# Kernel optimization log

Hardware: AMD Instinct MI355X
Metric: run time of the kernel (lower is better)

The kernel has to match this reference:

```python
import jax, jax.numpy as jnp
import numpy as np

B, T, C, H, N = 2, 2048, 2048, 32, 64
EPS_GN = 1e-5 * 8 ** 2  # eps * head_size_divisor^2


def _bf16(t):
    # kernel inputs are cast to bfloat16 in the original module
    return t.astype(jnp.bfloat16).astype(jnp.float32)


def _rwkv7_scan(r, k, v, w, a, b, s0):
    """Generalized delta-rule recurrence (fused_recurrent_rwkv7 semantics).
    r,k,v,w,a,b: [B,T,H,N]; s0: [B,H,N,N] with layout [key, value].
    S_t = diag(exp(w_t)) S + b_t (a_t^T S) + k_t v_t^T ; o_t = r_t^T S_t."""
    def step(S, ts):
        rt, kt, vt, wt, at, bt = ts  # each [B,H,N]
        sa = jnp.einsum('bhk,bhkv->bhv', at, S)
        S = S * jnp.exp(wt)[..., None] + bt[..., None] * sa[..., None, :] + kt[..., None] * vt[..., None, :]
        o = jnp.einsum('bhk,bhkv->bhv', rt, S)
        return S, o
    mv = lambda t: jnp.moveaxis(t, 1, 0)  # [B,T,H,N] -> [T,B,H,N]
    S, o = jax.lax.scan(step, s0, (mv(r), mv(k), mv(v), mv(w), mv(a), mv(b)))
    return jnp.moveaxis(o, 0, 1), S


def _forward(x, shift_state, wkv_state, v_first, x_r, x_w, x_k, x_v, x_a, x_g,
             w0, w1, w2, a0, a1, a2, v0, v1, v2, g1, g2, k_k, k_a, r_k,
             W_r, W_k, W_v, W_o, ln_w, ln_b):
    xx = jnp.concatenate([shift_state[:, None, :], x[:, :-1]], axis=1) - x
    xr, xw, xk, xv, xa, xg = (x + xx * m for m in (x_r, x_w, x_k, x_v, x_a, x_g))
    r = xr @ W_r
    w = -jax.nn.softplus(-(w0 + jnp.tanh(xw @ w1) @ w2)) - 0.5
    k = xk @ W_k
    v = xv @ W_v
    v = v + (v_first - v) * jax.nn.sigmoid(v0 + (xv @ v1) @ v2)  # layer_id > 0 branch
    a = jax.nn.sigmoid(a0 + (xa @ a1) @ a2)
    g = jax.nn.sigmoid(xg @ g1) @ g2
    kk = (k * k_k).reshape(B, T, H, N)
    kk = kk / jnp.maximum(jnp.linalg.norm(kk, axis=-1, keepdims=True), 1e-12)
    kk = kk.reshape(B, T, C)
    k = k * (1.0 + (a - 1.0) * k_a)
    hd = lambda t: _bf16(t).reshape(B, T, H, N)
    o, S = _rwkv7_scan(hd(r), hd(k), hd(v), hd(w), hd(-kk), hd(kk * a), wkv_state)
    y = o.reshape(B, T, H, N)
    # GroupNorm with H groups over C channels
    mu = y.mean(-1, keepdims=True)
    var = ((y - mu) ** 2).mean(-1, keepdims=True)
    y = ((y - mu) / jnp.sqrt(var + EPS_GN)).reshape(B, T, C) * ln_w + ln_b
    rr, k4, vv = r.reshape(B, T, H, N), k.reshape(B, T, H, N), v.reshape(B, T, H, N)
    y = y + ((rr * k4 * r_k).sum(-1, keepdims=True) * vv).reshape(B, T, C)
    out = (y * g) @ W_o
    return out, x[:, -1], S


def setup_inputs() -> dict:
    key = jax.random.key(0)
    ks = iter(jax.random.split(key, 40))
    rn = lambda shape, s=0.02: jax.random.normal(next(ks), shape, jnp.float32) * s
    ru = lambda shape: jax.random.uniform(next(ks), shape, jnp.float32)
    return dict(
        x=rn((B, T, C), 1.0), shift_state=rn((B, C), 1.0),
        wkv_state=jnp.zeros((B, H, N, N), jnp.float32), v_first=rn((B, T, C), 1.0),
        x_r=ru((1, 1, C)), x_w=ru((1, 1, C)), x_k=ru((1, 1, C)),
        x_v=ru((1, 1, C)), x_a=ru((1, 1, C)), x_g=ru((1, 1, C)),
        w0=rn((1, 1, C), 0.5) - 4.0, w1=rn((C, 64)), w2=rn((64, C)),
        a0=jnp.zeros((1, 1, C), jnp.float32), a1=rn((C, 64)), a2=rn((64, C)),
        v0=jnp.ones((1, 1, C), jnp.float32), v1=rn((C, 32)), v2=rn((32, C)),
        g1=rn((C, 128)), g2=rn((128, C)),
        k_k=jnp.full((1, 1, C), 0.85, jnp.float32), k_a=jnp.ones((1, 1, C), jnp.float32),
        r_k=rn((H, N), 0.1),
        W_r=rn((C, C), C ** -0.5), W_k=rn((C, C), C ** -0.5),
        W_v=rn((C, C), C ** -0.5), W_o=rn((C, C), C ** -0.5),
        ln_w=jnp.ones((C,), jnp.float32), ln_b=jnp.zeros((C,), jnp.float32))


def reference(x, shift_state, wkv_state, v_first, x_r, x_w, x_k, x_v, x_a, x_g,
              w0, w1, w2, a0, a1, a2, v0, v1, v2, g1, g2, k_k, k_a, r_k,
              W_r, W_k, W_v, W_o, ln_w, ln_b):
    return _forward(x, shift_state, wkv_state, v_first, x_r, x_w, x_k, x_v, x_a, x_g,
                    w0, w1, w2, a0, a1, a2, v0, v1, v2, g1, g2, k_k, k_a, r_k,
                    W_r, W_k, W_v, W_o, ln_w, ln_b)
```

## Files before the change

kernel.cpp:

```cpp
#include <hip/hip_runtime.h>
#include <cstdint>
#include <cmath>

#define B_ 2
#define T_ 2048
#define C_ 2048
#define H_ 32
#define BT_ (B_ * T_)
#define BTC_ ((size_t)B_ * T_ * C_)
#define L_ 128
#define NC_ 16

typedef __attribute__((ext_vector_type(4))) float f32x4;
typedef __attribute__((ext_vector_type(2))) float f32x2;
typedef __attribute__((ext_vector_type(8))) short bf16x8;
typedef __attribute__((ext_vector_type(4))) unsigned short us4;
typedef __attribute__((ext_vector_type(4))) int i32x4;

__device__ __forceinline__ unsigned short f2bf(float f) {
  union { float f; unsigned int u; } c; c.f = f;
  unsigned int u = c.u;
  return (unsigned short)((u + 0x7FFFu + ((u >> 16) & 1u)) >> 16);
}
__device__ __forceinline__ float bf2f(unsigned short h) {
  union { unsigned int u; float f; } c; c.u = ((unsigned int)h) << 16;
  return c.f;
}
__device__ __forceinline__ float rlane(float v, int lane) {
  return __int_as_float(__builtin_amdgcn_readlane(__float_as_int(v), lane));
}
__device__ __forceinline__ void split4(f32x4 v, us4& h, us4& l) {
  h.x = f2bf(v.x); l.x = f2bf(v.x - bf2f(h.x));
  h.y = f2bf(v.y); l.y = f2bf(v.y - bf2f(h.y));
  h.z = f2bf(v.z); l.z = f2bf(v.z - bf2f(h.z));
  h.w = f2bf(v.w); l.w = f2bf(v.w - bf2f(h.w));
}
__device__ __forceinline__ void g2l(const void* g, void* l) {
  __builtin_amdgcn_global_load_lds((const __attribute__((address_space(1))) void*)g,
                                   (__attribute__((address_space(3))) void*)l, 16, 0, 0);
}

__global__ __launch_bounds__(256) void k_mix(
    const float* __restrict__ x, const float* __restrict__ shift,
    const float* __restrict__ m_r, const float* __restrict__ m_w,
    const float* __restrict__ m_k, const float* __restrict__ m_v,
    const float* __restrict__ m_a, const float* __restrict__ m_g,
    unsigned short* __restrict__ r_h, unsigned short* __restrict__ r_l,
    unsigned short* __restrict__ k_h, unsigned short* __restrict__ k_l,
    unsigned short* __restrict__ v_h, unsigned short* __restrict__ v_l,
    unsigned short* __restrict__ o_w, unsigned short* __restrict__ o_a,
    unsigned short* __restrict__ o_g,
    float* __restrict__ xlast) {
  size_t i4 = ((size_t)blockIdx.x * 256 + threadIdx.x) * 4;
  int c = (int)(i4 % C_);
  size_t bt = i4 / C_;
  int t = (int)(bt % T_);
  int b = (int)(bt / T_);
  f32x4 xv = *(const f32x4*)(x + i4);
  f32x4 pv = (t == 0) ? *(const f32x4*)(shift + (size_t)b * C_ + c)
                      : *(const f32x4*)(x + i4 - C_);
  f32x4 dx = pv - xv;
#define MIXHL(mp, oh, ol) { f32x4 mm = *(const f32x4*)(mp + c); f32x4 rr = xv + dx * mm; \
    us4 hh, ll; split4(rr, hh, ll); *(us4*)(oh + i4) = hh; *(us4*)(ol + i4) = ll; }
#define MIXH(mp, oh) { f32x4 mm = *(const f32x4*)(mp + c); f32x4 rr = xv + dx * mm; \
    us4 pk; pk.x = f2bf(rr.x); pk.y = f2bf(rr.y); pk.z = f2bf(rr.z); pk.w = f2bf(rr.w); \
    *(us4*)(oh + i4) = pk; }
  MIXHL(m_r, r_h, r_l) MIXHL(m_k, k_h, k_l) MIXHL(m_v, v_h, v_l)
  MIXH(m_w, o_w) MIXH(m_a, o_a) MIXH(m_g, o_g)
#undef MIXHL
#undef MIXH
  if (t == T_ - 1) *(f32x4*)(xlast + (size_t)b * C_ + c) = xv;
}

__global__ __launch_bounds__(256) void k_tr(const float* __restrict__ in,
                                            unsigned short* __restrict__ out,
                                            int R, int Cc) {
  __shared__ float tile[32][33];
  int c0 = blockIdx.x * 32, r0 = blockIdx.y * 32;
  int tid = threadIdx.x;
  int rr = tid >> 3, c4 = (tid & 7) * 4;
  f32x4 v = *(const f32x4*)(in + (size_t)(r0 + rr) * Cc + c0 + c4);
  tile[rr][c4] = v.x; tile[rr][c4 + 1] = v.y; tile[rr][c4 + 2] = v.z; tile[rr][c4 + 3] = v.w;
  __syncthreads();
  int cc = tid >> 3, r4 = (tid & 7) * 4;
  us4 o;
  o.x = f2bf(tile[r4][cc]); o.y = f2bf(tile[r4 + 1][cc]);
  o.z = f2bf(tile[r4 + 2][cc]); o.w = f2bf(tile[r4 + 3][cc]);
  *(us4*)(out + (size_t)(c0 + cc) * R + r0 + r4) = o;
}

__global__ __launch_bounds__(256) void k_trs(const float* __restrict__ in,
                                             unsigned short* __restrict__ oh,
                                             unsigned short* __restrict__ ol,
                                             int R, int Cc) {
  __shared__ float tile[32][33];
  int c0 = blockIdx.x * 32, r0 = blockIdx.y * 32;
  int tid = threadIdx.x;
  int rr = tid >> 3, c4 = (tid & 7) * 4;
  f32x4 v = *(const f32x4*)(in + (size_t)(r0 + rr) * Cc + c0 + c4);
  tile[rr][c4] = v.x; tile[rr][c4 + 1] = v.y; tile[rr][c4 + 2] = v.z; tile[rr][c4 + 3] = v.w;
  __syncthreads();
  int cc = tid >> 3, r4 = (tid & 7) * 4;
  f32x4 w = { tile[r4][cc], tile[r4 + 1][cc], tile[r4 + 2][cc], tile[r4 + 3][cc] };
  us4 h, l; split4(w, h, l);
  size_t o = (size_t)(c0 + cc) * R + r0 + r4;
  *(us4*)(oh + o) = h; *(us4*)(ol + o) = l;
}

__global__ __launch_bounds__(256) void k_gemm(
    const unsigned short* __restrict__ X, const unsigned short* __restrict__ Wt,
    void* __restrict__ out, int M, int N, int K, int mode) {
  __shared__ alignas(16) unsigned short As[128 * 32];
  __shared__ alignas(16) unsigned short Bs[128 * 32];
  const int tid = threadIdx.x;
  const int lane = tid & 63, wave = tid >> 6;
  const int wr = wave >> 1, wc = wave & 1;
  const int lm = lane & 15, lq = lane >> 4;
  const int gx = gridDim.x;
  const int nwg = gx * gridDim.y;
  const int bid = blockIdx.y * gx + blockIdx.x;
  const int sz = (bid & 7) * (nwg >> 3) + (bid >> 3);
  const int m0 = (sz / gx) * 128, n0 = (sz % gx) * 128;
  const int srow = (lane >> 2);
  const int kcol = (lane & 3) * 8;
  f32x4 acc[4][4];
#pragma unroll
  for (int i = 0; i < 4; ++i)
#pragma unroll
    for (int j = 0; j < 4; ++j) acc[i][j] = (f32x4){0.f, 0.f, 0.f, 0.f};

  for (int k0 = 0; k0 < K; k0 += 32) {
#pragma unroll
    for (int p = 0; p < 2; ++p) {
      int row = wave * 32 + p * 16 + srow;
      g2l(X + (size_t)(m0 + row) * K + k0 + kcol, As + (wave * 2 + p) * 512);
      int n = n0 + row; if (n > N - 1) n = N - 1;
      g2l(Wt + (size_t)n * K + k0 + kcol, Bs + (wave * 2 + p) * 512);
    }
    __syncthreads();
    bf16x8 af[4], bfr[4];
#pragma unroll
    for (int i = 0; i < 4; ++i)
      af[i] = *(const bf16x8*)(As + (size_t)(wr * 64 + i * 16 + lm) * 32 + lq * 8);
#pragma unroll
    for (int j = 0; j < 4; ++j)
      bfr[j] = *(const bf16x8*)(Bs + (size_t)(wc * 64 + j * 16 + lm) * 32 + lq * 8);
#pragma unroll
    for (int i = 0; i < 4; ++i)
#pragma unroll
      for (int j = 0; j < 4; ++j)
        acc[i][j] = __builtin_amdgcn_mfma_f32_16x16x32_bf16(af[i], bfr[j], acc[i][j], 0, 0, 0);
    __syncthreads();
  }
#pragma unroll
  for (int i = 0; i < 4; ++i)
#pragma unroll
    for (int j = 0; j < 4; ++j) {
      int n = n0 + wc * 64 + j * 16 + lm;
      if (n >= N) continue;
      int mb = m0 + wr * 64 + i * 16 + lq * 4;
#pragma unroll
      for (int r = 0; r < 4; ++r) {
        float val = acc[i][j][r];
        size_t off = (size_t)(mb + r) * N + n;
        if (mode == 0) {
          ((float*)out)[off] = val;
        } else {
          if (mode == 2) val = tanhf(val);
          else if (mode == 3) val = 1.0f / (1.0f + __expf(-val));
          ((unsigned short*)out)[off] = f2bf(val);
        }
      }
    }
}

__global__ __launch_bounds__(256) void k_gemm2(
    const unsigned short* __restrict__ Xh, const unsigned short* __restrict__ Xl, int xlo,
    const unsigned short* __restrict__ Wh, const unsigned short* __restrict__ Wl, int wlo,
    void* __restrict__ out, int M, int N, int K, int mode) {
  __shared__ alignas(16) unsigned short Ah[128 * 32];
  __shared__ alignas(16) unsigned short Al[128 * 32];
  __shared__ alignas(16) unsigned short Bh[128 * 32];
  __shared__ alignas(16) unsigned short Bl[128 * 32];
  const int tid = threadIdx.x;
  const int lane = tid & 63, wave = tid >> 6;
  const int wr = wave >> 1, wc = wave & 1;
  const int lm = lane & 15, lq = lane >> 4;
  const int gx = gridDim.x;
  const int nwg = gx * gridDim.y;
  const int bid = blockIdx.y * gx + blockIdx.x;
  const int sz = (bid & 7) * (nwg >> 3) + (bid >> 3);
  const int m0 = (sz / gx) * 128, n0 = (sz % gx) * 128;
  const int srow = (lane >> 2);
  const int kcol = (lane & 3) * 8;
  f32x4 acc[4][4];
#pragma unroll
  for (int i = 0; i < 4; ++i)
#pragma unroll
    for (int j = 0; j < 4; ++j) acc[i][j] = (f32x4){0.f, 0.f, 0.f, 0.f};

  for (int k0 = 0; k0 < K; k0 += 32) {
#pragma unroll
    for (int p = 0; p < 2; ++p) {
      int row = wave * 32 + p * 16 + srow;
      int off = (wave * 2 + p) * 512;
      size_t ga = (size_t)(m0 + row) * K + k0 + kcol;
      g2l(Xh + ga, Ah + off);
      if (xlo) g2l(Xl + ga, Al + off);
      int n = n0 + row; if (n > N - 1) n = N - 1;
      size_t gb = (size_t)n * K + k0 + kcol;
      g2l(Wh + gb, Bh + off);
      if (wlo) g2l(Wl + gb, Bl + off);
    }
    __syncthreads();
    bf16x8 ah[4], bh[4];
#pragma unroll
    for (int i = 0; i < 4; ++i)
      ah[i] = *(const bf16x8*)(Ah + (size_t)(wr * 64 + i * 16 + lm) * 32 + lq * 8);
#pragma unroll
    for (int j = 0; j < 4; ++j)
      bh[j] = *(const bf16x8*)(Bh + (size_t)(wc * 64 + j * 16 + lm) * 32 + lq * 8);
#pragma unroll
    for (int i = 0; i < 4; ++i)
#pragma unroll
      for (int j = 0; j < 4; ++j)
        acc[i][j] = __builtin_amdgcn_mfma_f32_16x16x32_bf16(ah[i], bh[j], acc[i][j], 0, 0, 0);
    if (xlo) {
      bf16x8 al[4];
#pragma unroll
      for (int i = 0; i < 4; ++i)
        al[i] = *(const bf16x8*)(Al + (size_t)(wr * 64 + i * 16 + lm) * 32 + lq * 8);
#pragma unroll
      for (int i = 0; i < 4; ++i)
#pragma unroll
        for (int j = 0; j < 4; ++j)
          acc[i][j] = __builtin_amdgcn_mfma_f32_16x16x32_bf16(al[i], bh[j], acc[i][j], 0, 0, 0);
    }
    if (wlo) {
      bf16x8 bl[4];
#pragma unroll
      for (int j = 0; j < 4; ++j)
        bl[j] = *(const bf16x8*)(Bl + (size_t)(wc * 64 + j * 16 + lm) * 32 + lq * 8);
#pragma unroll
      for (int i = 0; i < 4; ++i)
#pragma unroll
        for (int j = 0; j < 4; ++j)
          acc[i][j] = __builtin_amdgcn_mfma_f32_16x16x32_bf16(ah[i], bl[j], acc[i][j], 0, 0, 0);
    }
    __syncthreads();
  }
#pragma unroll
  for (int i = 0; i < 4; ++i)
#pragma unroll
    for (int j = 0; j < 4; ++j) {
      int n = n0 + wc * 64 + j * 16 + lm;
      if (n >= N) continue;
      int mb = m0 + wr * 64 + i * 16 + lq * 4;
#pragma unroll
      for (int r = 0; r < 4; ++r) {
        float val = acc[i][j][r];
        size_t off = (size_t)(mb + r) * N + n;
        if (mode == 0) {
          ((float*)out)[off] = val;
        } else {
          if (mode == 2) val = tanhf(val);
          else if (mode == 3) val = 1.0f / (1.0f + __expf(-val));
          ((unsigned short*)out)[off] = f2bf(val);
        }
      }
    }
}

__global__ __launch_bounds__(256) void k_pre(
    const float* __restrict__ rp, const float* __restrict__ kp, float* __restrict__ vp,
    const unsigned short* __restrict__ ww, const unsigned short* __restrict__ aa,
    const unsigned short* __restrict__ vv,
    const float* __restrict__ vfirst,
    const float* __restrict__ w0, const float* __restrict__ a0, const float* __restrict__ v0,
    const float* __restrict__ kkc, const float* __restrict__ kac,
    const float* __restrict__ rkw,
    unsigned short* __restrict__ rb, unsigned short* __restrict__ wb,
    unsigned short* __restrict__ kb, unsigned short* __restrict__ vb,
    unsigned short* __restrict__ ab, unsigned short* __restrict__ bb,
    float* __restrict__ dp) {
  int gw = blockIdx.x * 4 + (threadIdx.x >> 6);
  int l = threadIdx.x & 63;
  int h = gw & (H_ - 1);
  size_t bt = (size_t)(gw >> 5);
  size_t idx = bt * C_ + h * 64 + l;
  int c = h * 64 + l;
  float rf = rp[idx], kf = kp[idx], vr = vp[idx];
  float z = -(w0[c] + bf2f(ww[idx]));
  float sp = (z > 15.f) ? z : log1pf(__expf(z));
  float wv = -sp - 0.5f;
  float ag = 1.f / (1.f + __expf(-(a0[c] + bf2f(aa[idx]))));
  float sv = 1.f / (1.f + __expf(-(v0[c] + bf2f(vv[idx]))));
  float vf = vr + (vfirst[idx] - vr) * sv;
  float kkv = kf * kkc[c];
  float ss = kkv * kkv;
#pragma unroll
  for (int m = 1; m < 64; m <<= 1) ss += __shfl_xor(ss, m);
  float nrm = fmaxf(sqrtf(ss), 1e-12f);
  float kkn = kkv / nrm;
  float ks = kf * (1.f + (ag - 1.f) * kac[c]);
  vp[idx] = vf;
  float bon = rf * ks * rkw[c];
#pragma unroll
  for (int m = 1; m < 64; m <<= 1) bon += __shfl_xor(bon, m);
  if (l == 0) dp[bt * H_ + h] = bon;
  rb[idx] = f2bf(rf); wb[idx] = f2bf(wv); kb[idx] = f2bf(ks);
  vb[idx] = f2bf(vf); ab[idx] = f2bf(-kkn); bb[idx] = f2bf(kkn * ag);
}

__global__ __launch_bounds__(64) void k_scanP(
    const unsigned short* __restrict__ rb,
    const unsigned short* __restrict__ wb, const unsigned short* __restrict__ kb,
    const unsigned short* __restrict__ vb, const unsigned short* __restrict__ ab,
    const unsigned short* __restrict__ bb,
    float* __restrict__ Pg, float* __restrict__ Ug,
    unsigned short* __restrict__ Zg, float* __restrict__ o) {
  const int blk = blockIdx.x;
  const int c = blk & (NC_ - 1), bh = blk >> 4;
  const int b = bh >> 5, h = bh & (H_ - 1);
  const int l = threadIdx.x & 63;
  size_t base = (size_t)b * ((size_t)T_ * C_) + (size_t)(c * L_) * C_ + h * 64 + l;
  size_t zbase = (size_t)blk * 8192;
  float P[64], U[64];
#pragma unroll
  for (int k = 0; k < 64; ++k) { P[k] = (k == l) ? 1.f : 0.f; U[k] = 0.f; }
  float pr[4], pw[4], pk[4], pv[4], pb[4], pa[4];
#pragma unroll
  for (int s = 0; s < 4; ++s) {
    size_t a_ = base + (size_t)s * C_;
    pr[s] = bf2f(rb[a_]); pw[s] = bf2f(wb[a_]); pk[s] = bf2f(kb[a_]);
    pv[s] = bf2f(vb[a_]); pb[s] = bf2f(bb[a_]);
    pa[s] = bf2f(ab[base + (size_t)(s + 1) * C_]);
  }
  float saP = bf2f(ab[base]), saU = 0.f;
  for (int t0 = 0; t0 < L_; t0 += 4) {
#pragma unroll
    for (int u = 0; u < 4; ++u) {
      const int t = t0 + u;
      float rl_ = pr[u], wl = pw[u], kl = pk[u], vl = pv[u], bl = pb[u], al = pa[u];
      if (t + 4 < L_) {
        size_t a_ = base + (size_t)(t + 4) * C_;
        pr[u] = bf2f(rb[a_]); pw[u] = bf2f(wb[a_]); pk[u] = bf2f(kb[a_]);
        pv[u] = bf2f(vb[a_]); pb[u] = bf2f(bb[a_]);
        int ta = t + 5; if (ta > L_ - 1) ta = L_ - 1;
        pa[u] = bf2f(ab[base + (size_t)ta * C_]);
      }
      float ew = exp2f(wl * 1.4426950408889634f);
      float zz0 = 0.f, zz1 = 0.f, zz2 = 0.f, zz3 = 0.f;
      float yy0 = 0.f, yy1 = 0.f, yy2 = 0.f, yy3 = 0.f;
      float qp0 = 0.f, qp1 = 0.f, qp2 = 0.f, qp3 = 0.f;
      float qu0 = 0.f, qu1 = 0.f, qu2 = 0.f, qu3 = 0.f;
#pragma unroll
      for (int k = 0; k < 64; k += 4) {
#define STEPK(kk, ZZ, YY, QP, QU)                                        \
        {                                                                \
          float s_ew = rlane(ew, kk), s_b = rlane(bl, kk),               \
                s_k = rlane(kl, kk);                                     \
          float Pn = fmaf(P[kk], s_ew, s_b * saP);                       \
          float Un = fmaf(U[kk], s_ew, fmaf(s_b, saU, s_k * vl));        \
          P[kk] = Pn; U[kk] = Un;                                        \
          float s_r = rlane(rl_, kk), s_a = rlane(al, kk);               \
          ZZ = fmaf(s_r, Pn, ZZ); YY = fmaf(s_r, Un, YY);                \
          QP = fmaf(s_a, Pn, QP); QU = fmaf(s_a, Un, QU);                \
        }
        STEPK(k,     zz0, yy0, qp0, qu0)
        STEPK(k + 1, zz1, yy1, qp1, qu1)
        STEPK(k + 2, zz2, yy2, qp2, qu2)
        STEPK(k + 3, zz3, yy3, qp3, qu3)
#undef STEPK
      }
      o[base + (size_t)t * C_] = (yy0 + yy1) + (yy2 + yy3);
      Zg[zbase + t * 64 + l] = f2bf((zz0 + zz1) + (zz2 + zz3));
      saP = (qp0 + qp1) + (qp2 + qp3);
      saU = (qu0 + qu1) + (qu2 + qu3);
    }
  }
  size_t pb_ = (size_t)blk * 4096;
#pragma unroll
  for (int k4 = 0; k4 < 64; k4 += 4) {
    f32x4 pv4 = { P[k4], P[k4 + 1], P[k4 + 2], P[k4 + 3] };
    *(f32x4*)(Pg + pb_ + (size_t)l * 64 + k4) = pv4;
  }
#pragma unroll
  for (int k = 0; k < 64; ++k) Ug[pb_ + (size_t)k * 64 + l] = U[k];
}

__global__ __launch_bounds__(256) void k_scanC(
    const float* __restrict__ Pg, const float* __restrict__ Ug,
    const float* __restrict__ s0, float* __restrict__ Scg, float* __restrict__ sout) {
  const int bh = blockIdx.x;
  const int l = threadIdx.x & 63;
  const int kg = __builtin_amdgcn_readfirstlane(threadIdx.x >> 6);
  const int kg16 = kg * 16;
  const int tid = threadIdx.x;
  __shared__ float Sb[4096];
#pragma unroll
  for (int q = 0; q < 4; ++q) {
    int e = tid * 16 + q * 4;
    *(f32x4*)(Sb + e) = *(const f32x4*)(s0 + (size_t)bh * 4096 + e);
  }
  __syncthreads();
  for (int c = 0; c < NC_; ++c) {
    size_t cb = ((size_t)bh * NC_ + c) * 4096;
#pragma unroll
    for (int q = 0; q < 4; ++q) {
      int e = tid * 16 + q * 4;
      *(f32x4*)(Scg + cb + e) = *(const f32x4*)(Sb + e);
    }
    const float* Pt = Pg + cb;
    const float* Uc = Ug + cb;
    float acc[16];
#pragma unroll
    for (int i = 0; i < 16; ++i) acc[i] = Uc[(size_t)(kg16 + i) * 64 + l];
    for (int j = 0; j < 64; ++j) {
      float s = Sb[j * 64 + l];
#pragma unroll
      for (int i = 0; i < 16; ++i) acc[i] = fmaf(Pt[j * 64 + kg16 + i], s, acc[i]);
    }
    __syncthreads();
#pragma unroll
    for (int i = 0; i < 16; ++i) Sb[(kg16 + i) * 64 + l] = acc[i];
    __syncthreads();
  }
#pragma unroll
  for (int q = 0; q < 4; ++q) {
    int e = tid * 16 + q * 4;
    *(f32x4*)(sout + (size_t)bh * 4096 + e) = *(const f32x4*)(Sb + e);
  }
}

__global__ __launch_bounds__(256) void k_scanO(
    const unsigned short* __restrict__ Zg, const float* __restrict__ Scg,
    float* __restrict__ o) {
  const int blk = blockIdx.x;
  const int c = blk & (NC_ - 1), bh = blk >> 4;
  const int b = bh >> 5, h = bh & (H_ - 1);
  const int l = threadIdx.x & 63;
  const int w = threadIdx.x >> 6;
  float S[64];
  const float* Sp = Scg + (size_t)blk * 4096 + l;
#pragma unroll
  for (int k = 0; k < 64; ++k) S[k] = Sp[(size_t)k * 64];
  size_t zb = (size_t)blk * 8192;
  size_t ob = (size_t)b * ((size_t)T_ * C_) + (size_t)(c * L_) * C_ + h * 64 + l;
  for (int tt = 0; tt < 32; ++tt) {
    int t = w * 32 + tt;
    float zv = bf2f(Zg[zb + t * 64 + l]);
    float a0_ = 0.f, a1_ = 0.f, a2_ = 0.f, a3_ = 0.f;
#pragma unroll
    for (int k = 0; k < 64; k += 4) {
      a0_ = fmaf(rlane(zv, k), S[k], a0_);
      a1_ = fmaf(rlane(zv, k + 1), S[k + 1], a1_);
      a2_ = fmaf(rlane(zv, k + 2), S[k + 2], a2_);
      a3_ = fmaf(rlane(zv, k + 3), S[k + 3], a3_);
    }
    o[ob + (size_t)t * C_] += (a0_ + a1_) + (a2_ + a3_);
  }
}

__global__ __launch_bounds__(256) void k_post(
    const float* __restrict__ o, const float* __restrict__ vp, const float* __restrict__ gp,
    const float* __restrict__ dp,
    const float* __restrict__ lnw, const float* __restrict__ lnb,
    unsigned short* __restrict__ z) {
  int gw = blockIdx.x * 4 + (threadIdx.x >> 6);
  int l = threadIdx.x & 63;
  int h = gw & (H_ - 1);
  size_t bt = (size_t)(gw >> 5);
  size_t idx = bt * C_ + h * 64 + l;
  int c = h * 64 + l;
  float ov = o[idx];
  float s1 = ov;
#pragma unroll
  for (int m = 1; m < 64; m <<= 1) s1 += __shfl_xor(s1, m);
  float mu = s1 * (1.f / 64.f);
  float d = ov - mu;
  float s2 = d * d;
#pragma unroll
  for (int m = 1; m < 64; m <<= 1) s2 += __shfl_xor(s2, m);
  float var = s2 * (1.f / 64.f);
  float y = d * rsqrtf(var + 6.4e-4f);
  y = y * lnw[c] + lnb[c];
  y = fmaf(dp[bt * H_ + h], vp[idx], y);
  z[idx] = f2bf(y * gp[idx]);
}

extern "C" void kernel_launch(void* const* d_in, const int* in_sizes, int n_in,
                              void* d_out, int out_size, void* d_ws, size_t ws_size,
                              hipStream_t stream) {
  const float* x      = (const float*)d_in[0];
  const float* shift  = (const float*)d_in[1];
  const float* wkv    = (const float*)d_in[2];
  const float* vfirst = (const float*)d_in[3];
  const float* x_r    = (const float*)d_in[4];
  const float* x_w    = (const float*)d_in[5];
  const float* x_k    = (const float*)d_in[6];
  const float* x_v    = (const float*)d_in[7];
  const float* x_a    = (const float*)d_in[8];
  const float* x_g    = (const float*)d_in[9];
  const float* w0     = (const float*)d_in[10];
  const float* w1     = (const float*)d_in[11];
  const float* w2     = (const float*)d_in[12];
  const float* a0     = (const float*)d_in[13];
  const float* a1     = (const float*)d_in[14];
  const float* a2     = (const float*)d_in[15];
  const float* v0     = (const float*)d_in[16];
  const float* v1     = (const float*)d_in[17];
  const float* v2     = (const float*)d_in[18];
  const float* g1     = (const float*)d_in[19];
  const float* g2     = (const float*)d_in[20];
  const float* k_k    = (const float*)d_in[21];
  const float* k_a    = (const float*)d_in[22];
  const float* r_k    = (const float*)d_in[23];
  const float* W_r    = (const float*)d_in[24];
  const float* W_k    = (const float*)d_in[25];
  const float* W_v    = (const float*)d_in[26];
  const float* W_o    = (const float*)d_in[27];
  const float* ln_w   = (const float*)d_in[28];
  const float* ln_b   = (const float*)d_in[29];

  char* wp = (char*)d_ws;
  auto alloc = [&](size_t bytes) { char* p = wp; wp += (bytes + 255) & ~(size_t)255; return p; };
  const size_t SB = BTC_ * 2;
  const size_t SF = BTC_ * 4;

  unsigned short* w1t = (unsigned short*)alloc((size_t)C_ * 64 * 2);
  unsigned short* w2t = (unsigned short*)alloc((size_t)C_ * 64 * 2);
  unsigned short* a1t = (unsigned short*)alloc((size_t)C_ * 64 * 2);
  unsigned short* a2t = (unsigned short*)alloc((size_t)C_ * 64 * 2);
  unsigned short* v1t = (unsigned short*)alloc((size_t)C_ * 32 * 2);
  unsigned short* v2t = (unsigned short*)alloc((size_t)C_ * 32 * 2);
  unsigned short* g1t = (unsigned short*)alloc((size_t)C_ * 128 * 2);
  unsigned short* g2t = (unsigned short*)alloc((size_t)C_ * 128 * 2);
  unsigned short* hw  = (unsigned short*)alloc((size_t)BT_ * 64 * 2);
  unsigned short* ha  = (unsigned short*)alloc((size_t)BT_ * 64 * 2);
  unsigned short* hv  = (unsigned short*)alloc((size_t)BT_ * 32 * 2);
  unsigned short* hg  = (unsigned short*)alloc((size_t)BT_ * 128 * 2);
  unsigned short* Wt2 = (unsigned short*)alloc((size_t)C_ * C_ * 2 * 2);
  float* dp           = (float*)alloc((size_t)BT_ * H_ * 4);
  unsigned short* xw  = (unsigned short*)alloc(SB);
  unsigned short* xa  = (unsigned short*)alloc(SB);
  unsigned short* xg  = (unsigned short*)alloc(SB);
  unsigned short* xr2 = (unsigned short*)alloc(2 * SB);
  unsigned short* xk2 = (unsigned short*)alloc(2 * SB);
  unsigned short* xv2 = (unsigned short*)alloc(2 * SB);
  float* rbuf         = (float*)alloc(SF);
  unsigned short* vbb = (unsigned short*)alloc(SB);

  unsigned short* Wh = Wt2;
  unsigned short* Wl = Wt2 + (size_t)C_ * C_;
  unsigned short* xr_h = xr2, *xr_l = xr2 + BTC_;
  unsigned short* xk_h = xk2, *xk_l = xk2 + BTC_;
  unsigned short* xv_h = xv2, *xv_l = xv2 + BTC_;
  float* kbuf = (float*)xr2;
  float* vbuf = (float*)xk2;
  unsigned short* rb = xv2;
  unsigned short* kb = xv2 + BTC_;
  float* gfull = rbuf;
  unsigned short* zbuf = (unsigned short*)xr2;
  float* Pg  = (float*)xr2;
  float* Ug  = Pg + (size_t)1024 * 4096;
  unsigned short* zg = Wt2;
  float* Scg = (float*)xw;

  float* outp  = (float*)d_out;
  float* xlast = outp + BTC_;
  float* soutp = outp + BTC_ + (size_t)B_ * C_;
  float* obuf  = outp;

  auto tr = [&](const float* in, unsigned short* out, int R, int Cc) {
    k_tr<<<dim3(Cc / 32, R / 32), 256, 0, stream>>>(in, out, R, Cc);
  };
  auto gemm = [&](const unsigned short* X, const unsigned short* Wtp, void* out,
                  int M, int N, int K, int mode) {
    k_gemm<<<dim3((N + 127) / 128, M / 128), 256, 0, stream>>>(X, Wtp, out, M, N, K, mode);
  };
  auto gemm2 = [&](const unsigned short* Xh_, const unsigned short* Xl_, int xlo,
                   const unsigned short* Wh_, const unsigned short* Wl_, int wlo,
                   void* out, int M, int N, int K, int mode) {
    k_gemm2<<<dim3((N + 127) / 128, M / 128), 256, 0, stream>>>(Xh_, Xl_, xlo, Wh_, Wl_, wlo,
                                                                out, M, N, K, mode);
  };

  k_mix<<<(int)(BTC_ / 4 / 256), 256, 0, stream>>>(x, shift, x_r, x_w, x_k, x_v, x_a, x_g,
                                                   xr_h, xr_l, xk_h, xk_l, xv_h, xv_l,
                                                   xw, xa, xg, xlast);
  tr(w1, w1t, C_, 64);  tr(w2, w2t, 64, C_);
  tr(a1, a1t, C_, 64);  tr(a2, a2t, 64, C_);
  tr(v1, v1t, C_, 32);  tr(v2, v2t, 32, C_);
  tr(g1, g1t, C_, 128); tr(g2, g2t, 128, C_);

  gemm(xw, w1t, hw, BT_, 64, C_, 2);
  gemm(xa, a1t, ha, BT_, 64, C_, 1);
  gemm2(xv_h, xv_l, 1, v1t, nullptr, 0, hv, BT_, 32, C_, 1);
  gemm(xg, g1t, hg, BT_, 128, C_, 3);

  k_trs<<<dim3(C_ / 32, C_ / 32), 256, 0, stream>>>(W_r, Wh, Wl, C_, C_);
  gemm2(xr_h, xr_l, 1, Wh, Wl, 1, rbuf, BT_, C_, C_, 0);
  k_trs<<<dim3(C_ / 32, C_ / 32), 256, 0, stream>>>(W_k, Wh, Wl, C_, C_);
  gemm2(xk_h, xk_l, 1, Wh, Wl, 1, kbuf, BT_, C_, C_, 0);
  k_trs<<<dim3(C_ / 32, C_ / 32), 256, 0, stream>>>(W_v, Wh, Wl, C_, C_);
  gemm2(xv_h, xv_l, 1, Wh, Wl, 1, vbuf, BT_, C_, C_, 0);

  gemm(hw, w2t, xw, BT_, C_, 64, 1);
  gemm(ha, a2t, xa, BT_, C_, 64, 1);
  gemm(hv, v2t, xg, BT_, C_, 32, 1);

  k_pre<<<BT_ * H_ / 4, 256, 0, stream>>>(rbuf, kbuf, vbuf, xw, xa, xg, vfirst,
                                          w0, a0, v0, k_k, k_a, r_k,
                                          rb, xw, kb, vbb, xa, xg, dp);

  gemm(hg, g2t, gfull, BT_, C_, 128, 0);

  k_scanP<<<B_ * H_ * NC_, 64, 0, stream>>>(rb, xw, kb, vbb, xa, xg, Pg, Ug, zg, obuf);
  k_scanC<<<B_ * H_, 256, 0, stream>>>(Pg, Ug, wkv, Scg, soutp);
  k_scanO<<<B_ * H_ * NC_, 256, 0, stream>>>(zg, Scg, obuf);

  k_post<<<BT_ * H_ / 4, 256, 0, stream>>>(obuf, vbuf, gfull, dp, ln_w, ln_b, zbuf);

  tr(W_o, Wh, C_, C_);
  gemm(zbuf, Wh, outp, BT_, C_, C_, 0);
}
```

Baseline: 1.408 ms.

## Halve scan chunk length, store P in bf16, split chunk combine across column blocks

```diff
diff --git a/kernel.cpp b/kernel.cpp
--- a/kernel.cpp
+++ b/kernel.cpp
@@ -8,8 +8,8 @@
 #define H_ 32
 #define BT_ (B_ * T_)
 #define BTC_ ((size_t)B_ * T_ * C_)
-#define L_ 128
-#define NC_ 16
+#define L_ 64
+#define NC_ 32
 
 typedef __attribute__((ext_vector_type(4))) float f32x4;
 typedef __attribute__((ext_vector_type(2))) float f32x2;
@@ -317,14 +317,14 @@
     const unsigned short* __restrict__ wb, const unsigned short* __restrict__ kb,
     const unsigned short* __restrict__ vb, const unsigned short* __restrict__ ab,
     const unsigned short* __restrict__ bb,
-    float* __restrict__ Pg, float* __restrict__ Ug,
+    unsigned short* __restrict__ Pg, float* __restrict__ Ug,
     unsigned short* __restrict__ Zg, float* __restrict__ o) {
   const int blk = blockIdx.x;
-  const int c = blk & (NC_ - 1), bh = blk >> 4;
+  const int c = blk & (NC_ - 1), bh = blk / NC_;
   const int b = bh >> 5, h = bh & (H_ - 1);
   const int l = threadIdx.x & 63;
   size_t base = (size_t)b * ((size_t)T_ * C_) + (size_t)(c * L_) * C_ + h * 64 + l;
-  size_t zbase = (size_t)blk * 8192;
+  size_t zbase = (size_t)blk * (L_ * 64);
   float P[64], U[64];
 #pragma unroll
   for (int k = 0; k < 64; ++k) { P[k] = (k == l) ? 1.f : 0.f; U[k] = 0.f; }
@@ -382,62 +382,79 @@
   size_t pb_ = (size_t)blk * 4096;
 #pragma unroll
   for (int k4 = 0; k4 < 64; k4 += 4) {
-    f32x4 pv4 = { P[k4], P[k4 + 1], P[k4 + 2], P[k4 + 3] };
-    *(f32x4*)(Pg + pb_ + (size_t)l * 64 + k4) = pv4;
+    us4 pk4;
+    pk4.x = f2bf(P[k4]); pk4.y = f2bf(P[k4 + 1]);
+    pk4.z = f2bf(P[k4 + 2]); pk4.w = f2bf(P[k4 + 3]);
+    *(us4*)(Pg + pb_ + (size_t)l * 64 + k4) = pk4;
   }
 #pragma unroll
   for (int k = 0; k < 64; ++k) Ug[pb_ + (size_t)k * 64 + l] = U[k];
 }
 
 __global__ __launch_bounds__(256) void k_scanC(
-    const float* __restrict__ Pg, const float* __restrict__ Ug,
+    const unsigned short* __restrict__ Pg, const float* __restrict__ Ug,
     const float* __restrict__ s0, float* __restrict__ Scg, float* __restrict__ sout) {
-  const int bh = blockIdx.x;
-  const int l = threadIdx.x & 63;
-  const int kg = __builtin_amdgcn_readfirstlane(threadIdx.x >> 6);
-  const int kg16 = kg * 16;
+  const int bh = blockIdx.x >> 2, q = blockIdx.x & 3;
   const int tid = threadIdx.x;
-  __shared__ float Sb[4096];
-#pragma unroll
-  for (int q = 0; q < 4; ++q) {
-    int e = tid * 16 + q * 4;
-    *(f32x4*)(Sb + e) = *(const f32x4*)(s0 + (size_t)bh * 4096 + e);
+  const int col = tid & 15;
+  const int r0 = (tid >> 4) * 4;
+  const int colg = q * 16 + col;
+  __shared__ float Sb[64][16];
+  __shared__ alignas(16) unsigned short Pb[4096];
+  float sreg[4];
+#pragma unroll
+  for (int rr = 0; rr < 4; ++rr) {
+    float v = s0[(size_t)bh * 4096 + (r0 + rr) * 64 + colg];
+    sreg[rr] = v; Sb[r0 + rr][col] = v;
+  }
+  {
+    size_t cb0 = ((size_t)bh * NC_) * 4096;
+    *(us4*)(Pb + tid * 16)      = *(const us4*)(Pg + cb0 + tid * 16);
+    *(us4*)(Pb + tid * 16 + 4)  = *(const us4*)(Pg + cb0 + tid * 16 + 4);
+    *(us4*)(Pb + tid * 16 + 8)  = *(const us4*)(Pg + cb0 + tid * 16 + 8);
+    *(us4*)(Pb + tid * 16 + 12) = *(const us4*)(Pg + cb0 + tid * 16 + 12);
   }
   __syncthreads();
   for (int c = 0; c < NC_; ++c) {
     size_t cb = ((size_t)bh * NC_ + c) * 4096;
 #pragma unroll
-    for (int q = 0; q < 4; ++q) {
-      int e = tid * 16 + q * 4;
-      *(f32x4*)(Scg + cb + e) = *(const f32x4*)(Sb + e);
-    }
-    const float* Pt = Pg + cb;
-    const float* Uc = Ug + cb;
-    float acc[16];
-#pragma unroll
-    for (int i = 0; i < 16; ++i) acc[i] = Uc[(size_t)(kg16 + i) * 64 + l];
+    for (int rr = 0; rr < 4; ++rr)
+      Scg[cb + (size_t)(r0 + rr) * 64 + colg] = sreg[rr];
+    float acc0 = Ug[cb + (size_t)r0 * 64 + colg];
+    float acc1 = Ug[cb + (size_t)(r0 + 1) * 64 + colg];
+    float acc2 = Ug[cb + (size_t)(r0 + 2) * 64 + colg];
+    float acc3 = Ug[cb + (size_t)(r0 + 3) * 64 + colg];
     for (int j = 0; j < 64; ++j) {
-      float s = Sb[j * 64 + l];
-#pragma unroll
-      for (int i = 0; i < 16; ++i) acc[i] = fmaf(Pt[j * 64 + kg16 + i], s, acc[i]);
+      float s = Sb[j][col];
+      us4 p4 = *(const us4*)(Pb + j * 64 + r0);
+      acc0 = fmaf(bf2f(p4.x), s, acc0);
+      acc1 = fmaf(bf2f(p4.y), s, acc1);
+      acc2 = fmaf(bf2f(p4.z), s, acc2);
+      acc3 = fmaf(bf2f(p4.w), s, acc3);
     }
     __syncthreads();
-#pragma unroll
-    for (int i = 0; i < 16; ++i) Sb[(kg16 + i) * 64 + l] = acc[i];
+    Sb[r0][col] = acc0; Sb[r0 + 1][col] = acc1;
+    Sb[r0 + 2][col] = acc2; Sb[r0 + 3][col] = acc3;
+    sreg[0] = acc0; sreg[1] = acc1; sreg[2] = acc2; sreg[3] = acc3;
+    if (c + 1 < NC_) {
+      size_t cbn = cb + 4096;
+      *(us4*)(Pb + tid * 16)      = *(const us4*)(Pg + cbn + tid * 16);
+      *(us4*)(Pb + tid * 16 + 4)  = *(const us4*)(Pg + cbn + tid * 16 + 4);
+      *(us4*)(Pb + tid * 16 + 8)  = *(const us4*)(Pg + cbn + tid * 16 + 8);
+      *(us4*)(Pb + tid * 16 + 12) = *(const us4*)(Pg + cbn + tid * 16 + 12);
+    }
     __syncthreads();
   }
 #pragma unroll
-  for (int q = 0; q < 4; ++q) {
-    int e = tid * 16 + q * 4;
-    *(f32x4*)(sout + (size_t)bh * 4096 + e) = *(const f32x4*)(Sb + e);
-  }
+  for (int rr = 0; rr < 4; ++rr)
+    sout[(size_t)bh * 4096 + (r0 + rr) * 64 + colg] = sreg[rr];
 }
 
 __global__ __launch_bounds__(256) void k_scanO(
     const unsigned short* __restrict__ Zg, const float* __restrict__ Scg,
     float* __restrict__ o) {
   const int blk = blockIdx.x;
-  const int c = blk & (NC_ - 1), bh = blk >> 4;
+  const int c = blk & (NC_ - 1), bh = blk / NC_;
   const int b = bh >> 5, h = bh & (H_ - 1);
   const int l = threadIdx.x & 63;
   const int w = threadIdx.x >> 6;
@@ -445,10 +462,10 @@
   const float* Sp = Scg + (size_t)blk * 4096 + l;
 #pragma unroll
   for (int k = 0; k < 64; ++k) S[k] = Sp[(size_t)k * 64];
-  size_t zb = (size_t)blk * 8192;
+  size_t zb = (size_t)blk * (L_ * 64);
   size_t ob = (size_t)b * ((size_t)T_ * C_) + (size_t)(c * L_) * C_ + h * 64 + l;
-  for (int tt = 0; tt < 32; ++tt) {
-    int t = w * 32 + tt;
+  for (int tt = 0; tt < L_ / 4; ++tt) {
+    int t = w * (L_ / 4) + tt;
     float zv = bf2f(Zg[zb + t * 64 + l]);
     float a0_ = 0.f, a1_ = 0.f, a2_ = 0.f, a3_ = 0.f;
 #pragma unroll
@@ -463,7 +480,8 @@
 }
 
 __global__ __launch_bounds__(256) void k_post(
-    const float* __restrict__ o, const float* __restrict__ vp, const float* __restrict__ gp,
+    const float* __restrict__ o, const float* __restrict__ vp,
+    const unsigned short* __restrict__ gp,
     const float* __restrict__ dp,
     const float* __restrict__ lnw, const float* __restrict__ lnb,
     unsigned short* __restrict__ z) {
@@ -486,7 +504,7 @@
   float y = d * rsqrtf(var + 6.4e-4f);
   y = y * lnw[c] + lnb[c];
   y = fmaf(dp[bt * H_ + h], vp[idx], y);
-  z[idx] = f2bf(y * gp[idx]);
+  z[idx] = f2bf(y * bf2f(gp[idx]));
 }
 
 extern "C" void kernel_launch(void* const* d_in, const int* in_sizes, int n_in,
@@ -560,10 +578,10 @@
   float* vbuf = (float*)xk2;
   unsigned short* rb = xv2;
   unsigned short* kb = xv2 + BTC_;
-  float* gfull = rbuf;
+  unsigned short* gb16 = (unsigned short*)rbuf;
+  unsigned short* Pgb  = (unsigned short*)rbuf + BTC_;
+  float* Ugf = (float*)xr2;
   unsigned short* zbuf = (unsigned short*)xr2;
-  float* Pg  = (float*)xr2;
-  float* Ug  = Pg + (size_t)1024 * 4096;
   unsigned short* zg = Wt2;
   float* Scg = (float*)xw;
 
@@ -614,13 +632,13 @@
                                           w0, a0, v0, k_k, k_a, r_k,
                                           rb, xw, kb, vbb, xa, xg, dp);
 
-  gemm(hg, g2t, gfull, BT_, C_, 128, 0);
-
-  k_scanP<<<B_ * H_ * NC_, 64, 0, stream>>>(rb, xw, kb, vbb, xa, xg, Pg, Ug, zg, obuf);
-  k_scanC<<<B_ * H_, 256, 0, stream>>>(Pg, Ug, wkv, Scg, soutp);
+  gemm(hg, g2t, gb16, BT_, C_, 128, 1);
+
+  k_scanP<<<B_ * H_ * NC_, 64, 0, stream>>>(rb, xw, kb, vbb, xa, xg, Pgb, Ugf, zg, obuf);
+  k_scanC<<<B_ * H_ * 4, 256, 0, stream>>>(Pgb, Ugf, wkv, Scg, soutp);
   k_scanO<<<B_ * H_ * NC_, 256, 0, stream>>>(zg, Scg, obuf);
 
-  k_post<<<BT_ * H_ / 4, 256, 0, stream>>>(obuf, vbuf, gfull, dp, ln_w, ln_b, zbuf);
+  k_post<<<BT_ * H_ / 4, 256, 0, stream>>>(obuf, vbuf, gb16, dp, ln_w, ln_b, zbuf);
 
   tr(W_o, Wh, C_, C_);
   gemm(zbuf, Wh, outp, BT_, C_, C_, 0);
```

New measurement: 1.379 ms. 2.1% less time.
